# Optimization experiments

Measured on AMD Instinct MI355X. Metric: run time of the kernel, lower is better.

## Reference

```python
import jax, jax.numpy as jnp
import numpy as np

PY_SIZES = [256, 64]
BASE = 256


def _resize_bilinear_ac(x, out):
    # NCHW bilinear resize, align_corners=True (matches F.interpolate(..., align_corners=True))
    def interp(x, axis, in_size):
        pos = jnp.arange(out, dtype=jnp.float32) * (in_size - 1) / (out - 1)
        lo = jnp.floor(pos).astype(jnp.int32)
        hi = jnp.minimum(lo + 1, in_size - 1)
        w = (pos - lo.astype(jnp.float32)).astype(x.dtype)
        shp = [1] * x.ndim
        shp[axis] = out
        w = w.reshape(shp)
        return jnp.take(x, lo, axis=axis) * (1 - w) + jnp.take(x, hi, axis=axis) * w
    x = interp(x, 2, x.shape[2])
    x = interp(x, 3, x.shape[3])
    return x


def _area_pool(x, f):
    # F.interpolate(mode='area') for integer downscale factor f == average pooling
    B, C, H, W = x.shape
    return x.reshape(B, C, H // f, f, W // f, f).mean(axis=(3, 5))


def _nearest_up_int(x, out):
    # F.interpolate(mode='nearest'): src = floor(dst * in/out)
    h = x.shape[2]
    idx = (jnp.arange(out) * h) // out
    return x[:, :, idx][:, :, :, idx]


def _buffers(B):
    grids, lin_ids, img_ids = [], [], []
    prev = 0
    for S in PY_SIZES:
        d = jnp.arange(S, dtype=jnp.float32) + 0.5
        gy, gx = jnp.meshgrid(d, d, indexing='ij')
        grids.append(jnp.broadcast_to(jnp.stack([gy, gx], -1)[None, None], (B, 1, S, S, 2)))
        lin_ids.append(jnp.arange(B * S * S, dtype=jnp.int32).reshape(B, 1, S, S) + prev)
        prev += B * S * S
        img_ids.append(jnp.broadcast_to(jnp.arange(B, dtype=jnp.float32)[:, None, None, None], (B, 1, S, S)))
    return grids, lin_ids, img_ids


def setup_inputs():
    key = jax.random.key(0)
    k1, k2 = jax.random.split(key)
    b_edges = (jax.random.uniform(k1, (64, 1, 512, 512)) < 0.08).astype(jnp.float32)
    sobel = jax.random.normal(k2, (64, 2, 512, 512), dtype=jnp.float32)
    return {"b_edges": b_edges, "sobel": sobel}


def reference(b_edges, sobel):
    B = b_edges.shape[0]
    grids, lin_ids, img_ids = _buffers(B)
    # resize post-Canny maps to base pyramid level
    e0 = jnp.clip(_resize_bilinear_ac(b_edges, BASE), 0, 1)
    s0 = _resize_bilinear_ac(sobel, BASE)
    py = [(e0, s0)]
    for S in PY_SIZES[1:]:
        f = BASE // S
        py.append((_area_pool(e0, f), _area_pool(s0, f)))
    p_lin, my_lin, centers, norms, sizes, imgid = [], [], [], [], [], []
    for i, (e, s) in enumerate(py):
        S = e.shape[2]
        idx = jnp.nonzero((e != 0).reshape(-1))[0]  # stream compaction of edge pixels
        if i + 1 < len(py):
            pl = _nearest_up_int(lin_ids[i + 1], S).reshape(-1)[idx]
        else:
            pl = lin_ids[i].reshape(-1)[idx]
        rat = BASE / S
        p_lin.append(pl)
        my_lin.append(lin_ids[i].reshape(-1)[idx])
        centers.append(grids[i].reshape(-1, 2)[idx] * rat)
        norms.append(jnp.transpose(s, (0, 2, 3, 1)).reshape(-1, 2)[idx])
        sizes.append(jnp.full(idx.shape, rat, dtype=jnp.float32))
        imgid.append(img_ids[i].reshape(-1)[idx])
    p_lin = jnp.concatenate(p_lin)
    my_lin = jnp.concatenate(my_lin)
    centers = jnp.concatenate(centers)
    norms = jnp.concatenate(norms)
    sizes = jnp.concatenate(sizes)
    imgid = jnp.concatenate(imgid)
    # parent scatter: linid -> row of that string, then gather by parent linid
    rowids = jnp.arange(my_lin.shape[0], dtype=jnp.int32)
    table = jnp.zeros(int(p_lin.max()) + 1, dtype=jnp.int32).at[my_lin].set(rowids)
    p_rowids = table[p_lin]
    norms = norms / jnp.linalg.norm(norms, axis=1, keepdims=True)
    # cross([nx,ny,0],[0,0,1]) = (ny,-nx,0)
    rt = jnp.stack([norms[:, 1], -norms[:, 0]], -1) * (sizes[:, None] / 2)
    locs_lf = centers + rt
    locs_rt = centers - rt
    return locs_lf, locs_rt, norms, sizes, centers, imgid, p_rowids, my_lin
```

## Files before the change

kernel.cpp:

```cpp
#include <hip/hip_runtime.h>
#include <math.h>

#define OFFSET1 4194304

__device__ __forceinline__ void ac_coef(int i, int& lo, int& hi, float& w) {
    float p = (float)(i * 511) / 255.0f;
    int l = (int)p;
    lo = l;
    hi = (l + 1 < 511) ? (l + 1) : 511;
    w = p - (float)l;
}

__device__ __forceinline__ float bilin(const float* __restrict__ img,
                                       int ly, int hy, float wy,
                                       int lx, int hx, float wx) {
    float a = img[ly * 512 + lx];
    float b = img[ly * 512 + hx];
    float c = img[hy * 512 + lx];
    float d = img[hy * 512 + hx];
    float rl = a * (1.0f - wy) + c * wy;
    float rh = b * (1.0f - wy) + d * wy;
    return rl * (1.0f - wx) + rh * wx;
}

__global__ __launch_bounds__(1024) void prep_kernel(const float* __restrict__ E,
                                                    const float* __restrict__ S,
                                                    float* __restrict__ s0,
                                                    float* __restrict__ s1,
                                                    unsigned long long* __restrict__ mask0,
                                                    unsigned long long* __restrict__ mask1,
                                                    int* __restrict__ counts0,
                                                    int* __restrict__ counts1,
                                                    int use_s0) {
    int tid = threadIdx.x;
    int blk = blockIdx.x;
    int b = blk >> 6, R = blk & 63;
    int r = tid >> 8, x = tid & 255;
    int y = 4 * R + r;
    int lane = tid & 63, wave = tid >> 6;

    int ly, hy, lx, hx; float wy, wx;
    ac_coef(y, ly, hy, wy);
    ac_coef(x, lx, hx, wx);

    const float* Eb = E + (size_t)b * 262144;
    bool pr = (bilin(Eb, ly, hy, wy, lx, hx, wx) != 0.0f);

    const float* Sb0 = S + (size_t)(b * 2 + 0) * 262144;
    const float* Sb1 = S + (size_t)(b * 2 + 1) * 262144;
    float v0 = bilin(Sb0, ly, hy, wy, lx, hx, wx);
    float v1 = bilin(Sb1, ly, hy, wy, lx, hx, wx);

    if (use_s0) {
        ((float2*)s0)[(size_t)(b * 256 + y) * 256 + x] = make_float2(v0, v1);
    }

    __shared__ int wc[16];
    unsigned long long m = __ballot(pr);
    if (lane == 0) {
        mask0[(size_t)b * 1024 + y * 4 + (x >> 6)] = m;
        wc[wave] = __popcll(m);
    }

    float h0 = v0 + __shfl_xor(v0, 1, 64); h0 += __shfl_xor(h0, 2, 64);
    float h1 = v1 + __shfl_xor(v1, 1, 64); h1 += __shfl_xor(h1, 2, 64);
    int   hp = pr ? 1 : 0;
    hp += __shfl_xor(hp, 1, 64); hp += __shfl_xor(hp, 2, 64);

    __shared__ float sA[4][64];
    __shared__ float sB[4][64];
    __shared__ int   sP[4][64];
    if ((x & 3) == 0) {
        int X = x >> 2;
        sA[r][X] = h0; sB[r][X] = h1; sP[r][X] = hp;
    }
    __syncthreads();

    if (tid < 64) {
        int X = tid;
        float a  = sA[0][X] + sA[1][X] + sA[2][X] + sA[3][X];
        float c2 = sB[0][X] + sB[1][X] + sB[2][X] + sB[3][X];
        int   pp = sP[0][X] + sP[1][X] + sP[2][X] + sP[3][X];
        bool p1 = (pp > 0);
        unsigned long long m1 = __ballot(p1);
        ((float2*)s1)[(size_t)blk * 64 + X] = make_float2(a * (1.0f / 16.0f),
                                                          c2 * (1.0f / 16.0f));
        if (tid == 0) { mask1[blk] = m1; counts1[blk] = __popcll(m1); }
    }
    if (tid == 0) {
        int t = 0;
        #pragma unroll
        for (int i = 0; i < 16; ++i) t += wc[i];
        counts0[blk] = t;
    }
}

__global__ __launch_bounds__(1024) void scan_kernel(const int* __restrict__ counts0,
                                                    int* __restrict__ offs0,
                                                    const int* __restrict__ counts1,
                                                    int* __restrict__ offs1,
                                                    int* __restrict__ totals) {
    __shared__ int wsum[16];
    int tid = threadIdx.x, lane = tid & 63, wave = tid >> 6;

    int carry = 0;
    for (int base = 0; base < 4096; base += 1024) {
        int v = counts0[base + tid];
        int inc = v;
        #pragma unroll
        for (int d = 1; d < 64; d <<= 1) {
            int t = __shfl_up(inc, (unsigned)d, 64);
            if (lane >= d) inc += t;
        }
        if (lane == 63) wsum[wave] = inc;
        __syncthreads();
        int wbase = 0;
        for (int i = 0; i < wave; ++i) wbase += wsum[i];
        int tot = 0;
        #pragma unroll
        for (int i = 0; i < 16; ++i) tot += wsum[i];
        offs0[base + tid] = carry + wbase + inc - v;
        carry += tot;
        __syncthreads();
    }
    if (tid == 0) totals[0] = carry;

    int carry1 = 0;
    for (int base = 0; base < 4096; base += 1024) {
        int v = counts1[base + tid];
        int inc = v;
        #pragma unroll
        for (int d = 1; d < 64; d <<= 1) {
            int t = __shfl_up(inc, (unsigned)d, 64);
            if (lane >= d) inc += t;
        }
        if (lane == 63) wsum[wave] = inc;
        __syncthreads();
        int wbase = 0;
        for (int i = 0; i < wave; ++i) wbase += wsum[i];
        int tot = 0;
        #pragma unroll
        for (int i = 0; i < 16; ++i) tot += wsum[i];
        offs1[base + tid] = carry1 + wbase + inc - v;
        carry1 += tot;
        __syncthreads();
    }
    if (tid == 0) totals[1] = carry1;
}

__device__ __forceinline__ void write_row(float* __restrict__ out, int N, int row,
                                          float cy, float cx, float s0v, float s1v,
                                          float half, float sz, float imgid,
                                          float prow, float mylin) {
    float len = sqrtf(s0v * s0v + s1v * s1v);
    float n0 = s0v / len, n1 = s1v / len;
    float rt0 = n1 * half, rt1 = -n0 * half;
    out[2 * row + 0] = cy + rt0;
    out[2 * row + 1] = cx + rt1;
    out[2 * N + 2 * row + 0] = cy - rt0;
    out[2 * N + 2 * row + 1] = cx - rt1;
    out[4 * N + 2 * row + 0] = n0;
    out[4 * N + 2 * row + 1] = n1;
    out[6 * N + row] = sz;
    out[7 * N + 2 * row + 0] = cy;
    out[7 * N + 2 * row + 1] = cx;
    out[9 * N + row] = imgid;
    out[10 * N + row] = prow;
    out[11 * N + row] = mylin;
}

__global__ __launch_bounds__(1024) void scatter1_kernel(const float* __restrict__ s1,
                                                        const unsigned long long* __restrict__ mask1,
                                                        const int* __restrict__ offs1,
                                                        const int* __restrict__ totals,
                                                        int* __restrict__ rank1,
                                                        float* __restrict__ out, int N) {
    int tid = threadIdx.x, lane = tid & 63, wave = tid >> 6;
    int g = blockIdx.x * 16 + wave;
    unsigned long long m = mask1[g];
    bool pr = (m >> lane) & 1ull;
    if (!pr) return;
    int row = totals[0] + offs1[g] + __popcll(m & ((1ull << lane) - 1ull));
    int q = g * 64 + lane;
    rank1[q] = row;
    float2 sv = ((const float2*)s1)[q];
    int b = g >> 6, Y = g & 63, X = lane;
    float cy = ((float)Y + 0.5f) * 4.0f;
    float cx = ((float)X + 0.5f) * 4.0f;
    write_row(out, N, row, cy, cx, sv.x, sv.y, 2.0f, 4.0f, (float)b,
              (float)row, (float)(OFFSET1 + q));
}

__global__ __launch_bounds__(1024) void scatter0_kernel(const float* __restrict__ S,
                                                        const float* __restrict__ s0,
                                                        const unsigned long long* __restrict__ mask0,
                                                        const int* __restrict__ offs0,
                                                        const int* __restrict__ rank1,
                                                        float* __restrict__ out, int N,
                                                        int use_s0) {
    int tid = threadIdx.x, lane = tid & 63, wave = tid >> 6;
    int blk = blockIdx.x;
    int b = blk >> 6, R = blk & 63;
    int r = tid >> 8, x = tid & 255;
    int y = 4 * R + r;
    int p = (b << 16) + (y << 8) + x;
    unsigned long long m = mask0[p >> 6];
    __shared__ int wc[16];
    if (lane == 0) wc[wave] = __popcll(m);
    __syncthreads();
    bool pr = (m >> lane) & 1ull;
    if (!pr) return;
    int wbase = 0;
    for (int i = 0; i < wave; ++i) wbase += wc[i];
    int row = offs0[blk] + wbase + __popcll(m & ((1ull << lane) - 1ull));

    float v0, v1;
    if (use_s0) {
        float2 sv = ((const float2*)s0)[(size_t)(b * 256 + y) * 256 + x];
        v0 = sv.x; v1 = sv.y;
    } else {
        int ly, hy, lx, hx; float wy, wx;
        ac_coef(y, ly, hy, wy);
        ac_coef(x, lx, hx, wx);
        v0 = bilin(S + (size_t)(b * 2 + 0) * 262144, ly, hy, wy, lx, hx, wx);
        v1 = bilin(S + (size_t)(b * 2 + 1) * 262144, ly, hy, wy, lx, hx, wx);
    }
    float cy = (float)y + 0.5f;
    float cx = (float)x + 0.5f;
    int parent = (b << 12) + ((y >> 2) << 6) + (x >> 2);
    write_row(out, N, row, cy, cx, v0, v1, 0.5f, 1.0f, (float)b,
              (float)rank1[parent], (float)p);
}

extern "C" void kernel_launch(void* const* d_in, const int* in_sizes, int n_in,
                              void* d_out, int out_size, void* d_ws, size_t ws_size,
                              hipStream_t stream) {
    const float* E = (const float*)d_in[0];
    const float* S = (const float*)d_in[1];
    float* out = (float*)d_out;
    int N = out_size / 12;

    char* ws = (char*)d_ws;
    int*  rank1   = (int*)ws;
    int*  counts0 = (int*)(ws + 1048576);
    int*  offs0   = counts0 + 4096;
    int*  counts1 = offs0 + 4096;
    int*  offs1   = counts1 + 4096;
    int*  totals  = offs1 + 4096;
    unsigned long long* mask0 = (unsigned long long*)(ws + 1048576 + 65536 + 64);
    unsigned long long* mask1 = mask0 + 65536;
    float* s1 = (float*)(mask1 + 4096);
    float* s0 = s1 + 524288;
    size_t need_with_s0 = (size_t)(s0 + 16777216 - (float*)ws) * sizeof(float) / sizeof(float);
    size_t base_bytes = (size_t)((char*)(s1 + 524288) - ws);
    int use_s0 = (ws_size >= base_bytes + 8388608ull * 8ull) ? 1 : 0;
    (void)need_with_s0;

    prep_kernel<<<4096, 1024, 0, stream>>>(E, S, use_s0 ? (float*)s0 : nullptr, s1,
                                           mask0, mask1, counts0, counts1, use_s0);
    scan_kernel<<<1, 1024, 0, stream>>>(counts0, offs0, counts1, offs1, totals);
    scatter1_kernel<<<256, 1024, 0, stream>>>(s1, mask1, offs1, totals, rank1, out, N);
    scatter0_kernel<<<4096, 1024, 0, stream>>>(S, (const float*)s0, mask0, offs0,
                                               rank1, out, N, use_s0);
}
```

Before: 93.88 us.

## Specialize bilinear prep to 2x stride with float4 loads and two pixels per thread

```diff
diff --git a/kernel.cpp b/kernel.cpp
--- a/kernel.cpp
+++ b/kernel.cpp
@@ -10,7 +10,6 @@
     hi = (l + 1 < 511) ? (l + 1) : 511;
     w = p - (float)l;
 }
-
 __device__ __forceinline__ float bilin(const float* __restrict__ img,
                                        int ly, int hy, float wy,
                                        int lx, int hx, float wx) {
@@ -23,56 +22,86 @@
     return rl * (1.0f - wx) + rh * wx;
 }
 
-__global__ __launch_bounds__(1024) void prep_kernel(const float* __restrict__ E,
-                                                    const float* __restrict__ S,
-                                                    float* __restrict__ s0,
-                                                    float* __restrict__ s1,
-                                                    unsigned long long* __restrict__ mask0,
-                                                    unsigned long long* __restrict__ mask1,
-                                                    int* __restrict__ counts0,
-                                                    int* __restrict__ counts1,
-                                                    int use_s0) {
+__device__ __forceinline__ unsigned long long expand_bits(unsigned long long x) {
+    x &= 0xFFFFFFFFull;
+    x = (x | (x << 16)) & 0x0000FFFF0000FFFFull;
+    x = (x | (x << 8))  & 0x00FF00FF00FF00FFull;
+    x = (x | (x << 4))  & 0x0F0F0F0F0F0F0F0Full;
+    x = (x | (x << 2))  & 0x3333333333333333ull;
+    x = (x | (x << 1))  & 0x5555555555555555ull;
+    return x;
+}
+
+__global__ __launch_bounds__(512) void prep_kernel(const float* __restrict__ E,
+                                                   const float* __restrict__ S,
+                                                   float* __restrict__ s0,
+                                                   float* __restrict__ s1,
+                                                   unsigned long long* __restrict__ mask0,
+                                                   unsigned long long* __restrict__ mask1,
+                                                   int* __restrict__ counts0,
+                                                   int* __restrict__ counts1,
+                                                   int use_s0) {
     int tid = threadIdx.x;
     int blk = blockIdx.x;
     int b = blk >> 6, R = blk & 63;
-    int r = tid >> 8, x = tid & 255;
+    int r = tid >> 7, xh = tid & 127;
     int y = 4 * R + r;
     int lane = tid & 63, wave = tid >> 6;
-
-    int ly, hy, lx, hx; float wy, wx;
-    ac_coef(y, ly, hy, wy);
-    ac_coef(x, lx, hx, wx);
-
-    const float* Eb = E + (size_t)b * 262144;
-    bool pr = (bilin(Eb, ly, hy, wy, lx, hx, wx) != 0.0f);
-
-    const float* Sb0 = S + (size_t)(b * 2 + 0) * 262144;
-    const float* Sb1 = S + (size_t)(b * 2 + 1) * 262144;
-    float v0 = bilin(Sb0, ly, hy, wy, lx, hx, wx);
-    float v1 = bilin(Sb1, ly, hy, wy, lx, hx, wx);
+    int half = wave & 1;
+
+    int ly = 2 * y;
+    float wy = (float)(y * 511) / 255.0f - (float)ly;
+    int x0 = 2 * xh;
+    float wx0 = (float)(x0 * 511) / 255.0f - (float)(4 * xh);
+    float wx1 = (float)((x0 + 1) * 511) / 255.0f - (float)(4 * xh + 2);
+
+    int off = b * 262144 + ly * 512 + 4 * xh;
+    float4 eL = *(const float4*)(E + off);
+    float4 eH = *(const float4*)(E + off + 512);
+    int offS = b * 524288 + ly * 512 + 4 * xh;
+    float4 aL = *(const float4*)(S + offS);
+    float4 aH = *(const float4*)(S + offS + 512);
+    float4 bL = *(const float4*)(S + offS + 262144);
+    float4 bH = *(const float4*)(S + offS + 262144 + 512);
+
+    float omwy = 1.0f - wy;
+    #define IPX(lo4a, lo4b, hi4a, hi4b, wx) \
+        ((lo4a * omwy + hi4a * wy) * (1.0f - wx) + (lo4b * omwy + hi4b * wy) * wx)
+    float e0v = IPX(eL.x, eL.y, eH.x, eH.y, wx0);
+    float e1v = IPX(eL.z, eL.w, eH.z, eH.w, wx1);
+    float v00 = IPX(aL.x, aL.y, aH.x, aH.y, wx0);
+    float v01 = IPX(aL.z, aL.w, aH.z, aH.w, wx1);
+    float v10 = IPX(bL.x, bL.y, bH.x, bH.y, wx0);
+    float v11 = IPX(bL.z, bL.w, bH.z, bH.w, wx1);
+    #undef IPX
+    bool pr0 = (e0v != 0.0f), pr1 = (e1v != 0.0f);
 
     if (use_s0) {
-        ((float2*)s0)[(size_t)(b * 256 + y) * 256 + x] = make_float2(v0, v1);
-    }
-
-    __shared__ int wc[16];
-    unsigned long long m = __ballot(pr);
+        ((float4*)s0)[(b * 256 + y) * 128 + xh] = make_float4(v00, v10, v01, v11);
+    }
+
+    __shared__ int wc[8];
+    unsigned long long mE = __ballot(pr0);
+    unsigned long long mO = __ballot(pr1);
     if (lane == 0) {
-        mask0[(size_t)b * 1024 + y * 4 + (x >> 6)] = m;
-        wc[wave] = __popcll(m);
-    }
-
-    float h0 = v0 + __shfl_xor(v0, 1, 64); h0 += __shfl_xor(h0, 2, 64);
-    float h1 = v1 + __shfl_xor(v1, 1, 64); h1 += __shfl_xor(h1, 2, 64);
-    int   hp = pr ? 1 : 0;
-    hp += __shfl_xor(hp, 1, 64); hp += __shfl_xor(hp, 2, 64);
+        int wbase = b * 1024 + y * 4 + 2 * half;
+        mask0[wbase]     = expand_bits(mE) | (expand_bits(mO) << 1);
+        mask0[wbase + 1] = expand_bits(mE >> 32) | (expand_bits(mO >> 32) << 1);
+        wc[wave] = __popcll(mE) + __popcll(mO);
+    }
+
+    float t0 = v00 + v01, t1 = v10 + v11;
+    int ip = (pr0 || pr1) ? 1 : 0;
+    float h0 = t0 + __shfl_xor(t0, 1, 64);
+    float h1 = t1 + __shfl_xor(t1, 1, 64);
+    ip |= __shfl_xor(ip, 1, 64);
 
     __shared__ float sA[4][64];
     __shared__ float sB[4][64];
     __shared__ int   sP[4][64];
-    if ((x & 3) == 0) {
-        int X = x >> 2;
-        sA[r][X] = h0; sB[r][X] = h1; sP[r][X] = hp;
+    if ((xh & 1) == 0) {
+        int X = (half << 5) + (lane >> 1);
+        sA[r][X] = h0; sB[r][X] = h1; sP[r][X] = ip;
     }
     __syncthreads();
 
@@ -80,17 +109,16 @@
         int X = tid;
         float a  = sA[0][X] + sA[1][X] + sA[2][X] + sA[3][X];
         float c2 = sB[0][X] + sB[1][X] + sB[2][X] + sB[3][X];
-        int   pp = sP[0][X] + sP[1][X] + sP[2][X] + sP[3][X];
-        bool p1 = (pp > 0);
+        bool p1 = (sP[0][X] | sP[1][X] | sP[2][X] | sP[3][X]) != 0;
         unsigned long long m1 = __ballot(p1);
-        ((float2*)s1)[(size_t)blk * 64 + X] = make_float2(a * (1.0f / 16.0f),
-                                                          c2 * (1.0f / 16.0f));
+        ((float2*)s1)[blk * 64 + X] = make_float2(a * (1.0f / 16.0f),
+                                                  c2 * (1.0f / 16.0f));
         if (tid == 0) { mask1[blk] = m1; counts1[blk] = __popcll(m1); }
     }
     if (tid == 0) {
         int t = 0;
         #pragma unroll
-        for (int i = 0; i < 16; ++i) t += wc[i];
+        for (int i = 0; i < 8; ++i) t += wc[i];
         counts0[blk] = t;
     }
 }
@@ -155,15 +183,11 @@
     float len = sqrtf(s0v * s0v + s1v * s1v);
     float n0 = s0v / len, n1 = s1v / len;
     float rt0 = n1 * half, rt1 = -n0 * half;
-    out[2 * row + 0] = cy + rt0;
-    out[2 * row + 1] = cx + rt1;
-    out[2 * N + 2 * row + 0] = cy - rt0;
-    out[2 * N + 2 * row + 1] = cx - rt1;
-    out[4 * N + 2 * row + 0] = n0;
-    out[4 * N + 2 * row + 1] = n1;
+    ((float2*)out)[row]           = make_float2(cy + rt0, cx + rt1);
+    ((float2*)(out + 2 * N))[row] = make_float2(cy - rt0, cx - rt1);
+    ((float2*)(out + 4 * N))[row] = make_float2(n0, n1);
     out[6 * N + row] = sz;
-    out[7 * N + 2 * row + 0] = cy;
-    out[7 * N + 2 * row + 1] = cx;
+    ((float2*)(out + 7 * N))[row] = make_float2(cy, cx);
     out[9 * N + row] = imgid;
     out[10 * N + row] = prow;
     out[11 * N + row] = mylin;
@@ -216,7 +240,7 @@
 
     float v0, v1;
     if (use_s0) {
-        float2 sv = ((const float2*)s0)[(size_t)(b * 256 + y) * 256 + x];
+        float2 sv = ((const float2*)s0)[(b * 256 + y) * 256 + x];
         v0 = sv.x; v1 = sv.y;
     } else {
         int ly, hy, lx, hx; float wy, wx;
@@ -251,13 +275,11 @@
     unsigned long long* mask1 = mask0 + 65536;
     float* s1 = (float*)(mask1 + 4096);
     float* s0 = s1 + 524288;
-    size_t need_with_s0 = (size_t)(s0 + 16777216 - (float*)ws) * sizeof(float) / sizeof(float);
     size_t base_bytes = (size_t)((char*)(s1 + 524288) - ws);
     int use_s0 = (ws_size >= base_bytes + 8388608ull * 8ull) ? 1 : 0;
-    (void)need_with_s0;
-
-    prep_kernel<<<4096, 1024, 0, stream>>>(E, S, use_s0 ? (float*)s0 : nullptr, s1,
-                                           mask0, mask1, counts0, counts1, use_s0);
+
+    prep_kernel<<<4096, 512, 0, stream>>>(E, S, (float*)s0, s1,
+                                          mask0, mask1, counts0, counts1, use_s0);
     scan_kernel<<<1, 1024, 0, stream>>>(counts0, offs0, counts1, offs1, totals);
     scatter1_kernel<<<256, 1024, 0, stream>>>(s1, mask1, offs1, totals, rank1, out, N);
     scatter0_kernel<<<4096, 1024, 0, stream>>>(S, (const float*)s0, mask0, offs0,
```

New measurement: 82.99 us. 1.13x faster.

## Restructure prep kernel so each lane handles a 4x4 tile with vectorized loads

Applied to the files above, without the earlier changes.

```diff
diff --git a/kernel.cpp b/kernel.cpp
--- a/kernel.cpp
+++ b/kernel.cpp
@@ -2,6 +2,8 @@
 #include <math.h>
 
 #define OFFSET1 4194304
+
+typedef unsigned long long u64;
 
 __device__ __forceinline__ void ac_coef(int i, int& lo, int& hi, float& w) {
     float p = (float)(i * 511) / 255.0f;
@@ -10,7 +12,6 @@
     hi = (l + 1 < 511) ? (l + 1) : 511;
     w = p - (float)l;
 }
-
 __device__ __forceinline__ float bilin(const float* __restrict__ img,
                                        int ly, int hy, float wy,
                                        int lx, int hx, float wx) {
@@ -23,75 +24,109 @@
     return rl * (1.0f - wx) + rh * wx;
 }
 
-__global__ __launch_bounds__(1024) void prep_kernel(const float* __restrict__ E,
-                                                    const float* __restrict__ S,
-                                                    float* __restrict__ s0,
-                                                    float* __restrict__ s1,
-                                                    unsigned long long* __restrict__ mask0,
-                                                    unsigned long long* __restrict__ mask1,
-                                                    int* __restrict__ counts0,
-                                                    int* __restrict__ counts1,
-                                                    int use_s0) {
-    int tid = threadIdx.x;
-    int blk = blockIdx.x;
-    int b = blk >> 6, R = blk & 63;
-    int r = tid >> 8, x = tid & 255;
-    int y = 4 * R + r;
-    int lane = tid & 63, wave = tid >> 6;
-
-    int ly, hy, lx, hx; float wy, wx;
-    ac_coef(y, ly, hy, wy);
-    ac_coef(x, lx, hx, wx);
-
-    const float* Eb = E + (size_t)b * 262144;
-    bool pr = (bilin(Eb, ly, hy, wy, lx, hx, wx) != 0.0f);
-
-    const float* Sb0 = S + (size_t)(b * 2 + 0) * 262144;
-    const float* Sb1 = S + (size_t)(b * 2 + 1) * 262144;
-    float v0 = bilin(Sb0, ly, hy, wy, lx, hx, wx);
-    float v1 = bilin(Sb1, ly, hy, wy, lx, hx, wx);
-
-    if (use_s0) {
-        ((float2*)s0)[(size_t)(b * 256 + y) * 256 + x] = make_float2(v0, v1);
-    }
-
-    __shared__ int wc[16];
-    unsigned long long m = __ballot(pr);
+__device__ __forceinline__ u64 expand4(unsigned v) {
+    u64 x = v & 0xFFFFu;
+    x = (x | (x << 24)) & 0x000000FF000000FFull;
+    x = (x | (x << 12)) & 0x000F000F000F000Full;
+    x = (x | (x << 6))  & 0x0303030303030303ull;
+    x = (x | (x << 3))  & 0x1111111111111111ull;
+    return x;
+}
+
+__global__ __launch_bounds__(256) void prep_kernel(const float* __restrict__ E,
+                                                   const float* __restrict__ S,
+                                                   float* __restrict__ s0,
+                                                   float* __restrict__ s1,
+                                                   u64* __restrict__ mask0,
+                                                   u64* __restrict__ mask1,
+                                                   int* __restrict__ counts0,
+                                                   int* __restrict__ counts1,
+                                                   int use_s0) {
+    int lane = threadIdx.x & 63;
+    int g = blockIdx.x * 4 + (threadIdx.x >> 6);
+    int b = g >> 6, R = g & 63;
+    int X = lane;
+
+    float wx[4], cwx[4];
+    #pragma unroll
+    for (int j = 0; j < 4; ++j) {
+        int xi = 4 * X + j;
+        wx[j] = (float)(xi * 511) / 255.0f - (float)(8 * X + 2 * j);
+        cwx[j] = 1.0f - wx[j];
+    }
+
+    unsigned pred = 0;
+    int rc = 0;
+    float acc0 = 0.0f, acc1 = 0.0f;
+    const float* Eb = E + b * 262144;
+    const float* Sp = S + (size_t)(b * 2) * 262144;
+
+    #pragma unroll
+    for (int r = 0; r < 4; ++r) {
+        int y = 4 * R + r, ly = 2 * y;
+        float wy = (float)(y * 511) / 255.0f - (float)ly;
+        float cwy = 1.0f - wy;
+
+        const float* Ep = Eb + ly * 512 + 8 * X;
+        float4 eA = *(const float4*)Ep;
+        float4 eB = *(const float4*)(Ep + 4);
+        float4 eC = *(const float4*)(Ep + 512);
+        float4 eD = *(const float4*)(Ep + 516);
+        const float* Sa = Sp + ly * 512 + 8 * X;
+        float4 a0 = *(const float4*)Sa;
+        float4 a1 = *(const float4*)(Sa + 4);
+        float4 a2 = *(const float4*)(Sa + 512);
+        float4 a3 = *(const float4*)(Sa + 516);
+        const float* Sb = Sa + 262144;
+        float4 q0 = *(const float4*)Sb;
+        float4 q1 = *(const float4*)(Sb + 4);
+        float4 q2 = *(const float4*)(Sb + 512);
+        float4 q3 = *(const float4*)(Sb + 516);
+
+        float e0 = (eA.x*cwy + eC.x*wy)*cwx[0] + (eA.y*cwy + eC.y*wy)*wx[0];
+        float e1 = (eA.z*cwy + eC.z*wy)*cwx[1] + (eA.w*cwy + eC.w*wy)*wx[1];
+        float e2 = (eB.x*cwy + eD.x*wy)*cwx[2] + (eB.y*cwy + eD.y*wy)*wx[2];
+        float e3 = (eB.z*cwy + eD.z*wy)*cwx[3] + (eB.w*cwy + eD.w*wy)*wx[3];
+        bool p0 = (e0 != 0.0f), p1 = (e1 != 0.0f), p2 = (e2 != 0.0f), p3 = (e3 != 0.0f);
+        pred |= (p0?1u:0u) << (4*r+0);
+        pred |= (p1?1u:0u) << (4*r+1);
+        pred |= (p2?1u:0u) << (4*r+2);
+        pred |= (p3?1u:0u) << (4*r+3);
+        u64 bl0 = __ballot(p0), bl1 = __ballot(p1), bl2 = __ballot(p2), bl3 = __ballot(p3);
+        rc += __popcll(bl0) + __popcll(bl1) + __popcll(bl2) + __popcll(bl3);
+        if (lane < 4) {
+            unsigned w0 = (unsigned)(bl0 >> (16 * lane)) & 0xFFFFu;
+            unsigned w1 = (unsigned)(bl1 >> (16 * lane)) & 0xFFFFu;
+            unsigned w2 = (unsigned)(bl2 >> (16 * lane)) & 0xFFFFu;
+            unsigned w3 = (unsigned)(bl3 >> (16 * lane)) & 0xFFFFu;
+            mask0[b * 1024 + y * 4 + lane] =
+                expand4(w0) | (expand4(w1) << 1) | (expand4(w2) << 2) | (expand4(w3) << 3);
+        }
+
+        float va0 = (a0.x*cwy + a2.x*wy)*cwx[0] + (a0.y*cwy + a2.y*wy)*wx[0];
+        float va1 = (a0.z*cwy + a2.z*wy)*cwx[1] + (a0.w*cwy + a2.w*wy)*wx[1];
+        float va2 = (a1.x*cwy + a3.x*wy)*cwx[2] + (a1.y*cwy + a3.y*wy)*wx[2];
+        float va3 = (a1.z*cwy + a3.z*wy)*cwx[3] + (a1.w*cwy + a3.w*wy)*wx[3];
+        float vb0 = (q0.x*cwy + q2.x*wy)*cwx[0] + (q0.y*cwy + q2.y*wy)*wx[0];
+        float vb1 = (q0.z*cwy + q2.z*wy)*cwx[1] + (q0.w*cwy + q2.w*wy)*wx[1];
+        float vb2 = (q1.x*cwy + q3.x*wy)*cwx[2] + (q1.y*cwy + q3.y*wy)*wx[2];
+        float vb3 = (q1.z*cwy + q3.z*wy)*cwx[3] + (q1.w*cwy + q3.w*wy)*wx[3];
+        acc0 += va0 + va1 + va2 + va3;
+        acc1 += vb0 + vb1 + vb2 + vb3;
+        if (use_s0) {
+            float4* dst = (float4*)s0 + (size_t)(b * 256 + y) * 128 + 2 * X;
+            dst[0] = make_float4(va0, vb0, va1, vb1);
+            dst[1] = make_float4(va2, vb2, va3, vb3);
+        }
+    }
+
+    u64 m1 = __ballot(pred != 0);
+    ((float2*)s1)[g * 64 + X] = make_float2(acc0 * (1.0f / 16.0f),
+                                            acc1 * (1.0f / 16.0f));
     if (lane == 0) {
-        mask0[(size_t)b * 1024 + y * 4 + (x >> 6)] = m;
-        wc[wave] = __popcll(m);
-    }
-
-    float h0 = v0 + __shfl_xor(v0, 1, 64); h0 += __shfl_xor(h0, 2, 64);
-    float h1 = v1 + __shfl_xor(v1, 1, 64); h1 += __shfl_xor(h1, 2, 64);
-    int   hp = pr ? 1 : 0;
-    hp += __shfl_xor(hp, 1, 64); hp += __shfl_xor(hp, 2, 64);
-
-    __shared__ float sA[4][64];
-    __shared__ float sB[4][64];
-    __shared__ int   sP[4][64];
-    if ((x & 3) == 0) {
-        int X = x >> 2;
-        sA[r][X] = h0; sB[r][X] = h1; sP[r][X] = hp;
-    }
-    __syncthreads();
-
-    if (tid < 64) {
-        int X = tid;
-        float a  = sA[0][X] + sA[1][X] + sA[2][X] + sA[3][X];
-        float c2 = sB[0][X] + sB[1][X] + sB[2][X] + sB[3][X];
-        int   pp = sP[0][X] + sP[1][X] + sP[2][X] + sP[3][X];
-        bool p1 = (pp > 0);
-        unsigned long long m1 = __ballot(p1);
-        ((float2*)s1)[(size_t)blk * 64 + X] = make_float2(a * (1.0f / 16.0f),
-                                                          c2 * (1.0f / 16.0f));
-        if (tid == 0) { mask1[blk] = m1; counts1[blk] = __popcll(m1); }
-    }
-    if (tid == 0) {
-        int t = 0;
-        #pragma unroll
-        for (int i = 0; i < 16; ++i) t += wc[i];
-        counts0[blk] = t;
+        counts0[g] = rc;
+        counts1[g] = __popcll(m1);
+        mask1[g] = m1;
     }
 }
 
@@ -155,29 +190,25 @@
     float len = sqrtf(s0v * s0v + s1v * s1v);
     float n0 = s0v / len, n1 = s1v / len;
     float rt0 = n1 * half, rt1 = -n0 * half;
-    out[2 * row + 0] = cy + rt0;
-    out[2 * row + 1] = cx + rt1;
-    out[2 * N + 2 * row + 0] = cy - rt0;
-    out[2 * N + 2 * row + 1] = cx - rt1;
-    out[4 * N + 2 * row + 0] = n0;
-    out[4 * N + 2 * row + 1] = n1;
+    ((float2*)out)[row]           = make_float2(cy + rt0, cx + rt1);
+    ((float2*)(out + 2 * N))[row] = make_float2(cy - rt0, cx - rt1);
+    ((float2*)(out + 4 * N))[row] = make_float2(n0, n1);
     out[6 * N + row] = sz;
-    out[7 * N + 2 * row + 0] = cy;
-    out[7 * N + 2 * row + 1] = cx;
+    ((float2*)(out + 7 * N))[row] = make_float2(cy, cx);
     out[9 * N + row] = imgid;
     out[10 * N + row] = prow;
     out[11 * N + row] = mylin;
 }
 
 __global__ __launch_bounds__(1024) void scatter1_kernel(const float* __restrict__ s1,
-                                                        const unsigned long long* __restrict__ mask1,
+                                                        const u64* __restrict__ mask1,
                                                         const int* __restrict__ offs1,
                                                         const int* __restrict__ totals,
                                                         int* __restrict__ rank1,
                                                         float* __restrict__ out, int N) {
     int tid = threadIdx.x, lane = tid & 63, wave = tid >> 6;
     int g = blockIdx.x * 16 + wave;
-    unsigned long long m = mask1[g];
+    u64 m = mask1[g];
     bool pr = (m >> lane) & 1ull;
     if (!pr) return;
     int row = totals[0] + offs1[g] + __popcll(m & ((1ull << lane) - 1ull));
@@ -193,7 +224,7 @@
 
 __global__ __launch_bounds__(1024) void scatter0_kernel(const float* __restrict__ S,
                                                         const float* __restrict__ s0,
-                                                        const unsigned long long* __restrict__ mask0,
+                                                        const u64* __restrict__ mask0,
                                                         const int* __restrict__ offs0,
                                                         const int* __restrict__ rank1,
                                                         float* __restrict__ out, int N,
@@ -204,7 +235,7 @@
     int r = tid >> 8, x = tid & 255;
     int y = 4 * R + r;
     int p = (b << 16) + (y << 8) + x;
-    unsigned long long m = mask0[p >> 6];
+    u64 m = mask0[p >> 6];
     __shared__ int wc[16];
     if (lane == 0) wc[wave] = __popcll(m);
     __syncthreads();
@@ -216,7 +247,7 @@
 
     float v0, v1;
     if (use_s0) {
-        float2 sv = ((const float2*)s0)[(size_t)(b * 256 + y) * 256 + x];
+        float2 sv = ((const float2*)s0)[(b * 256 + y) * 256 + x];
         v0 = sv.x; v1 = sv.y;
     } else {
         int ly, hy, lx, hx; float wy, wx;
@@ -247,17 +278,15 @@
     int*  counts1 = offs0 + 4096;
     int*  offs1   = counts1 + 4096;
     int*  totals  = offs1 + 4096;
-    unsigned long long* mask0 = (unsigned long long*)(ws + 1048576 + 65536 + 64);
-    unsigned long long* mask1 = mask0 + 65536;
+    u64*  mask0   = (u64*)(ws + 1048576 + 65536 + 64);
+    u64*  mask1   = mask0 + 65536;
     float* s1 = (float*)(mask1 + 4096);
     float* s0 = s1 + 524288;
-    size_t need_with_s0 = (size_t)(s0 + 16777216 - (float*)ws) * sizeof(float) / sizeof(float);
     size_t base_bytes = (size_t)((char*)(s1 + 524288) - ws);
     int use_s0 = (ws_size >= base_bytes + 8388608ull * 8ull) ? 1 : 0;
-    (void)need_with_s0;
-
-    prep_kernel<<<4096, 1024, 0, stream>>>(E, S, use_s0 ? (float*)s0 : nullptr, s1,
-                                           mask0, mask1, counts0, counts1, use_s0);
+
+    prep_kernel<<<1024, 256, 0, stream>>>(E, S, (float*)s0, s1,
+                                          mask0, mask1, counts0, counts1, use_s0);
     scan_kernel<<<1, 1024, 0, stream>>>(counts0, offs0, counts1, offs1, totals);
     scatter1_kernel<<<256, 1024, 0, stream>>>(s1, mask1, offs1, totals, rank1, out, N);
     scatter0_kernel<<<4096, 1024, 0, stream>>>(S, (const float*)s0, mask0, offs0,
```

Measured after the change: 83.16 us. 11.4% less time.
